# Kernel tuning notes

Hardware: AMD Instinct MI355X
Metric: run time of the kernel (lower is better)

Reference implementation:

```python
import jax, jax.numpy as jnp
import numpy as np

N, K, C = 128, 64, 64

def _w(key, shape, scale):
    return (jax.random.normal(key, shape, dtype=jnp.float32) * scale)

def setup_inputs() -> dict:
    key = jax.random.key(0)
    ks = jax.random.split(key, 20)
    s1 = 1.0 / np.sqrt(C)
    s2 = 1.0 / np.sqrt(2 * C)
    inp = {
        "x": jax.random.normal(ks[0], (N, K, C), dtype=jnp.float32),
        "W_lin": _w(ks[1], (C, C), s1), "b_lin": jnp.zeros((C,), jnp.float32),
        # unary_passing: Linear(C,C) -> tanh -> Linear(C,C)
        "Wu1": _w(ks[2], (C, C), s1), "bu1": jnp.zeros((C,), jnp.float32),
        "Wu2": _w(ks[3], (C, C), s1), "bu2": jnp.zeros((C,), jnp.float32),
        # unary_gate: Linear(C,C) -> tanh -> Linear(C,C) -> sigmoid
        "Wug1": _w(ks[4], (C, C), s1), "bug1": jnp.zeros((C,), jnp.float32),
        "Wug2": _w(ks[5], (C, C), s1), "bug2": jnp.zeros((C,), jnp.float32),
        # binary_passing: Linear(2C,C) -> tanh -> Linear(C,C)
        "Wb1": _w(ks[6], (2 * C, C), s2), "bb1": jnp.zeros((C,), jnp.float32),
        "Wb2": _w(ks[7], (C, C), s1), "bb2": jnp.zeros((C,), jnp.float32),
        # binary_gate: Linear(2C,C) -> tanh -> Linear(C,C) -> sigmoid
        "Wbg1": _w(ks[8], (2 * C, C), s2), "bbg1": jnp.zeros((C,), jnp.float32),
        "Wbg2": _w(ks[9], (C, C), s1), "bbg2": jnp.zeros((C,), jnp.float32),
        "t": 0,  # time scalar, ignored by IgnoreLinear base layer
    }
    return inp


def reference(x, W_lin, b_lin, Wu1, bu1, Wu2, bu2, Wug1, bug1, Wug2, bug2,
              Wb1, bb1, Wb2, bb2, Wbg1, bbg1, Wbg2, bbg2, t):
    # base linear map (IgnoreLinear: ignores t)
    h = x @ W_lin + b_lin                          # (N, K, C)
    n, k, c = h.shape
    # unary message with gate
    um = jnp.tanh(h @ Wu1 + bu1) @ Wu2 + bu2
    ug = jax.nn.sigmoid(jnp.tanh(h @ Wug1 + bug1) @ Wug2 + bug2)
    um = um * ug                                   # (N, K, C)
    # all-pairs broadcast-concat: hm[n,i,j] = [h[n,j], h[n,i]]
    hm = jnp.concatenate([
        jnp.broadcast_to(h[:, None, :, :], (n, k, k, c)),
        jnp.broadcast_to(h[:, :, None, :], (n, k, k, c)),
    ], axis=3)                                     # (N, K, K, 2C)
    bm = jnp.tanh(hm @ Wb1 + bb1) @ Wb2 + bb2      # (N, K, K, C)
    bg = jax.nn.sigmoid(jnp.tanh(hm @ Wbg1 + bbg1) @ Wbg2 + bbg2)
    # sum over axis 1 (includes diagonal, as in original), normalize by K-1
    bm = jnp.sum(bm * bg, axis=1) / jnp.float32(k - 1)  # (N, K, C)
    return um + bm
```

## Files before the change

kernel.cpp:

```cpp
#include <hip/hip_runtime.h>

#define S_ELEM 524288
#define WST 72

typedef __attribute__((ext_vector_type(4))) float    f32x4;
typedef __attribute__((ext_vector_type(2))) float    f32x2;
typedef __attribute__((ext_vector_type(8))) _Float16 f16x8;
typedef __attribute__((ext_vector_type(2))) _Float16 f16x2;

__device__ __forceinline__ float rcp_f(float x) { return __builtin_amdgcn_rcpf(x); }
__device__ __forceinline__ float fast_sigmoid(float x) {
    return rcp_f(1.0f + __expf(-x));
}
__device__ __forceinline__ float tanh_exp(float x) {
    return 1.0f - 2.0f * rcp_f(__expf(2.0f * x) + 1.0f);
}

__device__ __forceinline__ void read_afrag(const _Float16* Act, int row, int qd,
                                           f16x8 a[2]) {
    a[0] = *(const f16x8*)(Act + row * WST + qd * 8);
    a[1] = *(const f16x8*)(Act + row * WST + 32 + qd * 8);
}

__device__ __forceinline__ void mfma_gemm(const f16x8 a[2], const _Float16* Wt,
                                          int l16, int qd, f32x4 acc[4]) {
#pragma unroll
    for (int cc = 0; cc < 4; ++cc) {
        const _Float16* wr = Wt + (cc * 16 + l16) * WST + qd * 8;
        f16x8 b0 = *(const f16x8*)(wr);
        f16x8 b1 = *(const f16x8*)(wr + 32);
        acc[cc] = __builtin_amdgcn_mfma_f32_16x16x32_f16(a[0], b0, acc[cc], 0, 0, 0);
        acc[cc] = __builtin_amdgcn_mfma_f32_16x16x32_f16(a[1], b1, acc[cc], 0, 0, 0);
    }
}

__device__ __forceinline__ void stage_weight(const float* __restrict__ W,
                                             _Float16* Wt, int tid) {
#pragma unroll
    for (int i = 0; i < 16; ++i) {
        int idx = tid + i * 256;
        int k = idx >> 6, n = idx & 63;
        Wt[n * WST + k] = (_Float16)W[idx];
    }
}

__global__ __launch_bounds__(256) void fused_prep_kernel(
    const float* __restrict__ x,
    const float* __restrict__ W_lin, const float* __restrict__ b_lin,
    const float* __restrict__ Wu1,  const float* __restrict__ bu1,
    const float* __restrict__ Wu2,  const float* __restrict__ bu2,
    const float* __restrict__ Wug1, const float* __restrict__ bug1,
    const float* __restrict__ Wug2, const float* __restrict__ bug2,
    const float* __restrict__ Wb1,  const float* __restrict__ bb1,
    const float* __restrict__ Wbg1, const float* __restrict__ bbg1,
    const float* __restrict__ Wb2,  const float* __restrict__ Wbg2,
    float* __restrict__ EP,  float* __restrict__ EQ,
    float* __restrict__ EPg, float* __restrict__ EQg,
    float* __restrict__ um,  _Float16* __restrict__ wfrag)
{
    int tid = threadIdx.x;

    if (blockIdx.x >= 128) {
        int base = (blockIdx.x - 128) * 1024 + tid * 4;
#pragma unroll
        for (int u = 0; u < 4; ++u) {
            int idx = base + u;
            const float* W = (idx < 4096) ? Wb2 : Wbg2;
            int r = idx & 4095;
            int jj = r & 7, l16 = (r >> 3) & 15, qd = (r >> 7) & 3;
            int kk = (r >> 9) & 1, cc = (r >> 10) & 3;
            int k = kk * 32 + qd * 8 + jj, col = cc * 16 + l16;
            wfrag[idx] = (_Float16)W[k * 64 + col];
        }
        return;
    }

    __shared__ _Float16 Wt0[64 * WST], Wt1[64 * WST];
    __shared__ _Float16 Ax[64 * WST], Ah[64 * WST], Au[64 * WST], Agg[64 * WST];

    int w = tid >> 6, l = tid & 63, qd = l >> 4, l16 = l & 15;
    int row0 = blockIdx.x * 64;
    int myrow = 16 * w + l16;
    int orow  = 16 * w + qd * 4;

#pragma unroll
    for (int i = 0; i < 8; ++i) {
        int e = tid * 2 + i * 512;
        f32x2 v = *(const f32x2*)(x + (size_t)row0 * 64 + e);
        f16x2 p;
        p[0] = (_Float16)v[0];
        p[1] = (_Float16)v[1];
        *(f16x2*)(Ax + (e >> 6) * WST + (e & 63)) = p;
    }
    stage_weight(W_lin, Wt0, tid);
    __syncthreads();

    f32x4 acc[4];

    {
        f16x8 a[2]; read_afrag(Ax, myrow, qd, a);
#pragma unroll
        for (int cc = 0; cc < 4; ++cc) {
            float bv = b_lin[cc * 16 + l16];
            acc[cc] = (f32x4){bv, bv, bv, bv};
        }
        mfma_gemm(a, Wt0, l16, qd, acc);
#pragma unroll
        for (int cc = 0; cc < 4; ++cc)
#pragma unroll
            for (int r = 0; r < 4; ++r)
                Ah[(orow + r) * WST + cc * 16 + l16] = (_Float16)acc[cc][r];
    }
    stage_weight(Wb1, Wt1, tid);
    __syncthreads();

    f16x8 ah[2]; read_afrag(Ah, myrow, qd, ah);

#define STAGE(WTBUF, BIAS, NEXT_W, NEXT_BUF, EMIT)                         \
    {                                                                      \
        _Pragma("unroll")                                                  \
        for (int cc = 0; cc < 4; ++cc) {                                   \
            float bv = (BIAS) ? (BIAS)[cc * 16 + l16] : 0.0f;              \
            acc[cc] = (f32x4){bv, bv, bv, bv};                             \
        }                                                                  \
        mfma_gemm(ah, WTBUF, l16, qd, acc);                                \
        EMIT                                                               \
        if (NEXT_W) stage_weight(NEXT_W, NEXT_BUF, tid);                   \
        __syncthreads();                                                   \
    }

#define EMIT_EXP(DST)                                                      \
        _Pragma("unroll")                                                  \
        for (int cc = 0; cc < 4; ++cc)                                     \
            _Pragma("unroll")                                              \
            for (int r = 0; r < 4; ++r)                                    \
                DST[(size_t)(row0 + orow + r) * 64 + cc * 16 + l16] =      \
                    __expf(2.0f * acc[cc][r]);

#define EMIT_TANH(DST)                                                     \
        _Pragma("unroll")                                                  \
        for (int cc = 0; cc < 4; ++cc)                                     \
            _Pragma("unroll")                                              \
            for (int r = 0; r < 4; ++r)                                    \
                DST[(orow + r) * WST + cc * 16 + l16] =                    \
                    (_Float16)tanh_exp(acc[cc][r]);

    STAGE(Wt1, bb1,  Wb1 + 4096,  Wt0, EMIT_EXP(EP))
    STAGE(Wt0, (const float*)nullptr, Wbg1, Wt1, EMIT_EXP(EQ))
    STAGE(Wt1, bbg1, Wbg1 + 4096, Wt0, EMIT_EXP(EPg))
    STAGE(Wt0, (const float*)nullptr, Wu1,  Wt1, EMIT_EXP(EQg))
    STAGE(Wt1, bu1,  Wug1, Wt0, EMIT_TANH(Au))
    STAGE(Wt0, bug1, Wu2,  Wt1, EMIT_TANH(Agg))

    f32x4 uacc[4];
    {
        f16x8 au[2]; read_afrag(Au, myrow, qd, au);
#pragma unroll
        for (int cc = 0; cc < 4; ++cc) {
            float bv = bu2[cc * 16 + l16];
            uacc[cc] = (f32x4){bv, bv, bv, bv};
        }
        mfma_gemm(au, Wt1, l16, qd, uacc);
    }
    stage_weight(Wug2, Wt0, tid);
    __syncthreads();

    {
        f16x8 ag[2]; read_afrag(Agg, myrow, qd, ag);
#pragma unroll
        for (int cc = 0; cc < 4; ++cc) {
            float bv = bug2[cc * 16 + l16];
            acc[cc] = (f32x4){bv, bv, bv, bv};
        }
        mfma_gemm(ag, Wt0, l16, qd, acc);
#pragma unroll
        for (int cc = 0; cc < 4; ++cc)
#pragma unroll
            for (int r = 0; r < 4; ++r)
                um[(size_t)(row0 + orow + r) * 64 + cc * 16 + l16] =
                    uacc[cc][r] * fast_sigmoid(acc[cc][r]);
    }
#undef STAGE
#undef EMIT_EXP
#undef EMIT_TANH
}

__global__ __launch_bounds__(512) void binary_kernel(
    const float* __restrict__ EP,  const float* __restrict__ EQ,
    const float* __restrict__ EPg, const float* __restrict__ EQg,
    const float* __restrict__ bb2, const float* __restrict__ bbg2,
    const _Float16* __restrict__ wfrag,
    const float* __restrict__ um, float* __restrict__ out)
{
    __shared__ float Qb[8192];
    float* Qs  = Qb;
    float* Qgs = Qb + 4096;

    int tid = threadIdx.x, w = tid >> 6, l = tid & 63;
    int qd = l >> 4, l16 = l & 15;
    int n = blockIdx.y, j0 = blockIdx.x * 16;

    const float* EQn  = EQ  + (size_t)n * 4096;
    const float* EQgn = EQg + (size_t)n * 4096;
    for (int idx = tid * 4; idx < 4096; idx += 2048) {
        *(f32x4*)(Qs + idx)  = *(const f32x4*)(EQn + idx);
        *(f32x4*)(Qgs + idx) = *(const f32x4*)(EQgn + idx);
    }

    const float* Pr  = EP  + (size_t)n * 4096 + (j0 + l16) * 64;
    const float* Pgr = EPg + (size_t)n * 4096 + (j0 + l16) * 64;
    f32x4 pm[4], pg[4];
    pm[0] = *(const f32x4*)(Pr + qd * 8);
    pm[1] = *(const f32x4*)(Pr + qd * 8 + 4);
    pm[2] = *(const f32x4*)(Pr + 32 + qd * 8);
    pm[3] = *(const f32x4*)(Pr + 32 + qd * 8 + 4);
    pg[0] = *(const f32x4*)(Pgr + qd * 8);
    pg[1] = *(const f32x4*)(Pgr + qd * 8 + 4);
    pg[2] = *(const f32x4*)(Pgr + 32 + qd * 8);
    pg[3] = *(const f32x4*)(Pgr + 32 + qd * 8 + 4);

    const f16x8* wf = (const f16x8*)wfrag;
    f16x8 bwm[4][2], bwg[4][2];
#pragma unroll
    for (int cc = 0; cc < 4; ++cc)
#pragma unroll
        for (int kk = 0; kk < 2; ++kk) {
            bwm[cc][kk] = wf[cc * 128 + kk * 64 + qd * 16 + l16];
            bwg[cc][kk] = wf[512 + cc * 128 + kk * 64 + qd * 16 + l16];
        }
    float bim[4], big[4];
#pragma unroll
    for (int cc = 0; cc < 4; ++cc) {
        bim[cc] = bb2[cc * 16 + l16];
        big[cc] = bbg2[cc * 16 + l16];
    }
    f32x4 acc[4];
#pragma unroll
    for (int cc = 0; cc < 4; ++cc) acc[cc] = (f32x4){0.f, 0.f, 0.f, 0.f};
    __syncthreads();

    for (int ii = 8 * w; ii < 8 * w + 8; ++ii) {
        const float* qm = Qs  + ii * 64;
        const float* qg = Qgs + ii * 64;
        f16x8 am[2], ag[2];
#pragma unroll
        for (int kk = 0; kk < 2; ++kk) {
            int cb = kk * 32 + qd * 8;
            f32x4 qa = *(const f32x4*)(qm + cb);
            f32x4 qb = *(const f32x4*)(qm + cb + 4);
            f32x4 ha = *(const f32x4*)(qg + cb);
            f32x4 hb = *(const f32x4*)(qg + cb + 4);
#pragma unroll
            for (int t = 0; t < 4; ++t) {
                am[kk][t]     = (_Float16)(1.0f - 2.0f * rcp_f(__builtin_fmaf(pm[kk*2][t],   qa[t], 1.0f)));
                am[kk][t + 4] = (_Float16)(1.0f - 2.0f * rcp_f(__builtin_fmaf(pm[kk*2+1][t], qb[t], 1.0f)));
                ag[kk][t]     = (_Float16)(1.0f - 2.0f * rcp_f(__builtin_fmaf(pg[kk*2][t],   ha[t], 1.0f)));
                ag[kk][t + 4] = (_Float16)(1.0f - 2.0f * rcp_f(__builtin_fmaf(pg[kk*2+1][t], hb[t], 1.0f)));
            }
        }
#pragma unroll
        for (int cc = 0; cc < 4; ++cc) {
            f32x4 d = {bim[cc], bim[cc], bim[cc], bim[cc]};
            d = __builtin_amdgcn_mfma_f32_16x16x32_f16(am[0], bwm[cc][0], d, 0, 0, 0);
            d = __builtin_amdgcn_mfma_f32_16x16x32_f16(am[1], bwm[cc][1], d, 0, 0, 0);
            f32x4 e = {big[cc], big[cc], big[cc], big[cc]};
            e = __builtin_amdgcn_mfma_f32_16x16x32_f16(ag[0], bwg[cc][0], e, 0, 0, 0);
            e = __builtin_amdgcn_mfma_f32_16x16x32_f16(ag[1], bwg[cc][1], e, 0, 0, 0);
#pragma unroll
            for (int r = 0; r < 4; ++r)
                acc[cc][r] += d[r] * fast_sigmoid(e[r]);
        }
    }

    __syncthreads();
    float* Red = Qb;
#pragma unroll
    for (int cc = 0; cc < 4; ++cc)
#pragma unroll
        for (int r = 0; r < 4; ++r)
            Red[w * 1024 + (qd * 4 + r) * 64 + cc * 16 + l16] = acc[cc][r];
    __syncthreads();

    {
        int flat = tid * 2;
        f32x2 s = {0.f, 0.f};
#pragma unroll
        for (int ww = 0; ww < 8; ++ww)
            s += *(const f32x2*)(Red + ww * 1024 + flat);
        int row = flat >> 6, col = flat & 63;
        size_t g = (size_t)n * 4096 + (size_t)(j0 + row) * 64 + col;
        f32x2 u = *(const f32x2*)(um + g);
        f32x2 o;
        o[0] = u[0] + s[0] * (1.0f / 63.0f);
        o[1] = u[1] + s[1] * (1.0f / 63.0f);
        *(f32x2*)(out + g) = o;
    }
}

extern "C" void kernel_launch(void* const* d_in, const int* in_sizes, int n_in,
                              void* d_out, int out_size, void* d_ws, size_t ws_size,
                              hipStream_t stream)
{
    (void)in_sizes; (void)n_in; (void)out_size; (void)ws_size;
    const float* x     = (const float*)d_in[0];
    const float* W_lin = (const float*)d_in[1];
    const float* b_lin = (const float*)d_in[2];
    const float* Wu1   = (const float*)d_in[3];
    const float* bu1   = (const float*)d_in[4];
    const float* Wu2   = (const float*)d_in[5];
    const float* bu2   = (const float*)d_in[6];
    const float* Wug1  = (const float*)d_in[7];
    const float* bug1  = (const float*)d_in[8];
    const float* Wug2  = (const float*)d_in[9];
    const float* bug2  = (const float*)d_in[10];
    const float* Wb1   = (const float*)d_in[11];
    const float* bb1   = (const float*)d_in[12];
    const float* Wb2   = (const float*)d_in[13];
    const float* bb2   = (const float*)d_in[14];
    const float* Wbg1  = (const float*)d_in[15];
    const float* bbg1  = (const float*)d_in[16];
    const float* Wbg2  = (const float*)d_in[17];
    const float* bbg2  = (const float*)d_in[18];

    float*    ws    = (float*)d_ws;
    _Float16* wfrag = (_Float16*)ws;
    float* base = ws + 4096;
    float* EP   = base;
    float* EQ   = base + 1 * (size_t)S_ELEM;
    float* EPg  = base + 2 * (size_t)S_ELEM;
    float* EQg  = base + 3 * (size_t)S_ELEM;
    float* um   = base + 4 * (size_t)S_ELEM;

    hipLaunchKernelGGL(fused_prep_kernel, dim3(136), dim3(256), 0, stream,
        x, W_lin, b_lin, Wu1, bu1, Wu2, bu2, Wug1, bug1, Wug2, bug2,
        Wb1, bb1, Wbg1, bbg1, Wb2, Wbg2,
        EP, EQ, EPg, EQg, um, wfrag);
    hipLaunchKernelGGL(binary_kernel, dim3(4, 128), dim3(512), 0, stream,
        EP, EQ, EPg, EQg, bb2, bbg2, wfrag, um, (float*)d_out);
}
```

Measured before the change: 134.5 us.

## Fuse prep and binary kernels into one per-batch kernel with LDS intermediates

Merges the two-kernel pipeline into a single kernel. Each block handles one batch element and half of the output rows, recomputes the per-row linear, unary and binary projections, and keeps EP/EQ/um in shared memory instead of writing them to global workspace and reading them back. This removes a launch, the global round trip of several MB of intermediates, and the separate weight-fragment pass. In exchange, each batch's prep GEMMs are computed twice (once per block), the grid drops to 256 blocks of 512 threads, and about 111 KB of LDS per block may limit occupancy.

```diff
diff --git a/kernel.cpp b/kernel.cpp
--- a/kernel.cpp
+++ b/kernel.cpp
@@ -1,6 +1,5 @@
 #include <hip/hip_runtime.h>
 
-#define S_ELEM 524288
 #define WST 72
 
 typedef __attribute__((ext_vector_type(4))) float    f32x4;
@@ -16,35 +15,32 @@
     return 1.0f - 2.0f * rcp_f(__expf(2.0f * x) + 1.0f);
 }
 
-__device__ __forceinline__ void read_afrag(const _Float16* Act, int row, int qd,
-                                           f16x8 a[2]) {
-    a[0] = *(const f16x8*)(Act + row * WST + qd * 8);
-    a[1] = *(const f16x8*)(Act + row * WST + 32 + qd * 8);
-}
-
-__device__ __forceinline__ void mfma_gemm(const f16x8 a[2], const _Float16* Wt,
-                                          int l16, int qd, f32x4 acc[4]) {
-#pragma unroll
-    for (int cc = 0; cc < 4; ++cc) {
-        const _Float16* wr = Wt + (cc * 16 + l16) * WST + qd * 8;
+__device__ __forceinline__ void stage512(const float* __restrict__ W,
+                                         _Float16* Wt, int tid) {
+#pragma unroll
+    for (int i = 0; i < 8; ++i) {
+        int idx = tid + i * 512;
+        int k = idx >> 6, c = idx & 63;
+        Wt[c * WST + k] = (_Float16)W[idx];
+    }
+}
+
+__device__ __forceinline__ void gemm2(const _Float16* Act, int arow, int qd,
+                                      const _Float16* Wt, int colb,
+                                      f32x4 acc[2]) {
+    f16x8 a0 = *(const f16x8*)(Act + arow * WST + qd * 8);
+    f16x8 a1 = *(const f16x8*)(Act + arow * WST + 32 + qd * 8);
+#pragma unroll
+    for (int cc = 0; cc < 2; ++cc) {
+        const _Float16* wr = Wt + (colb + cc * 16) * WST + qd * 8;
         f16x8 b0 = *(const f16x8*)(wr);
         f16x8 b1 = *(const f16x8*)(wr + 32);
-        acc[cc] = __builtin_amdgcn_mfma_f32_16x16x32_f16(a[0], b0, acc[cc], 0, 0, 0);
-        acc[cc] = __builtin_amdgcn_mfma_f32_16x16x32_f16(a[1], b1, acc[cc], 0, 0, 0);
-    }
-}
-
-__device__ __forceinline__ void stage_weight(const float* __restrict__ W,
-                                             _Float16* Wt, int tid) {
-#pragma unroll
-    for (int i = 0; i < 16; ++i) {
-        int idx = tid + i * 256;
-        int k = idx >> 6, n = idx & 63;
-        Wt[n * WST + k] = (_Float16)W[idx];
-    }
-}
-
-__global__ __launch_bounds__(256) void fused_prep_kernel(
+        acc[cc] = __builtin_amdgcn_mfma_f32_16x16x32_f16(a0, b0, acc[cc], 0, 0, 0);
+        acc[cc] = __builtin_amdgcn_mfma_f32_16x16x32_f16(a1, b1, acc[cc], 0, 0, 0);
+    }
+}
+
+__global__ __launch_bounds__(512, 2) void fused_all_kernel(
     const float* __restrict__ x,
     const float* __restrict__ W_lin, const float* __restrict__ b_lin,
     const float* __restrict__ Wu1,  const float* __restrict__ bu1,
@@ -52,181 +48,181 @@
     const float* __restrict__ Wug1, const float* __restrict__ bug1,
     const float* __restrict__ Wug2, const float* __restrict__ bug2,
     const float* __restrict__ Wb1,  const float* __restrict__ bb1,
+    const float* __restrict__ Wb2,  const float* __restrict__ bb2,
     const float* __restrict__ Wbg1, const float* __restrict__ bbg1,
-    const float* __restrict__ Wb2,  const float* __restrict__ Wbg2,
-    float* __restrict__ EP,  float* __restrict__ EQ,
-    float* __restrict__ EPg, float* __restrict__ EQg,
-    float* __restrict__ um,  _Float16* __restrict__ wfrag)
+    const float* __restrict__ Wbg2, const float* __restrict__ bbg2,
+    float* __restrict__ out)
 {
-    int tid = threadIdx.x;
-
-    if (blockIdx.x >= 128) {
-        int base = (blockIdx.x - 128) * 1024 + tid * 4;
-#pragma unroll
-        for (int u = 0; u < 4; ++u) {
-            int idx = base + u;
-            const float* W = (idx < 4096) ? Wb2 : Wbg2;
-            int r = idx & 4095;
-            int jj = r & 7, l16 = (r >> 3) & 15, qd = (r >> 7) & 3;
-            int kk = (r >> 9) & 1, cc = (r >> 10) & 3;
-            int k = kk * 32 + qd * 8 + jj, col = cc * 16 + l16;
-            wfrag[idx] = (_Float16)W[k * 64 + col];
-        }
-        return;
-    }
-
-    __shared__ _Float16 Wt0[64 * WST], Wt1[64 * WST];
-    __shared__ _Float16 Ax[64 * WST], Ah[64 * WST], Au[64 * WST], Agg[64 * WST];
-
-    int w = tid >> 6, l = tid & 63, qd = l >> 4, l16 = l & 15;
-    int row0 = blockIdx.x * 64;
-    int myrow = 16 * w + l16;
-    int orow  = 16 * w + qd * 4;
-
-#pragma unroll
-    for (int i = 0; i < 8; ++i) {
-        int e = tid * 2 + i * 512;
-        f32x2 v = *(const f32x2*)(x + (size_t)row0 * 64 + e);
-        f16x2 p;
-        p[0] = (_Float16)v[0];
-        p[1] = (_Float16)v[1];
-        *(f16x2*)(Ax + (e >> 6) * WST + (e & 63)) = p;
-    }
-    stage_weight(W_lin, Wt0, tid);
-    __syncthreads();
-
-    f32x4 acc[4];
-
-    {
-        f16x8 a[2]; read_afrag(Ax, myrow, qd, a);
-#pragma unroll
-        for (int cc = 0; cc < 4; ++cc) {
-            float bv = b_lin[cc * 16 + l16];
-            acc[cc] = (f32x4){bv, bv, bv, bv};
-        }
-        mfma_gemm(a, Wt0, l16, qd, acc);
-#pragma unroll
-        for (int cc = 0; cc < 4; ++cc)
-#pragma unroll
-            for (int r = 0; r < 4; ++r)
-                Ah[(orow + r) * WST + cc * 16 + l16] = (_Float16)acc[cc][r];
-    }
-    stage_weight(Wb1, Wt1, tid);
-    __syncthreads();
-
-    f16x8 ah[2]; read_afrag(Ah, myrow, qd, ah);
-
-#define STAGE(WTBUF, BIAS, NEXT_W, NEXT_BUF, EMIT)                         \
-    {                                                                      \
-        _Pragma("unroll")                                                  \
-        for (int cc = 0; cc < 4; ++cc) {                                   \
-            float bv = (BIAS) ? (BIAS)[cc * 16 + l16] : 0.0f;              \
-            acc[cc] = (f32x4){bv, bv, bv, bv};                             \
-        }                                                                  \
-        mfma_gemm(ah, WTBUF, l16, qd, acc);                                \
-        EMIT                                                               \
-        if (NEXT_W) stage_weight(NEXT_W, NEXT_BUF, tid);                   \
-        __syncthreads();                                                   \
-    }
-
-#define EMIT_EXP(DST)                                                      \
-        _Pragma("unroll")                                                  \
-        for (int cc = 0; cc < 4; ++cc)                                     \
-            _Pragma("unroll")                                              \
-            for (int r = 0; r < 4; ++r)                                    \
-                DST[(size_t)(row0 + orow + r) * 64 + cc * 16 + l16] =      \
-                    __expf(2.0f * acc[cc][r]);
-
-#define EMIT_TANH(DST)                                                     \
-        _Pragma("unroll")                                                  \
-        for (int cc = 0; cc < 4; ++cc)                                     \
-            _Pragma("unroll")                                              \
-            for (int r = 0; r < 4; ++r)                                    \
-                DST[(orow + r) * WST + cc * 16 + l16] =                    \
-                    (_Float16)tanh_exp(acc[cc][r]);
-
-    STAGE(Wt1, bb1,  Wb1 + 4096,  Wt0, EMIT_EXP(EP))
-    STAGE(Wt0, (const float*)nullptr, Wbg1, Wt1, EMIT_EXP(EQ))
-    STAGE(Wt1, bbg1, Wbg1 + 4096, Wt0, EMIT_EXP(EPg))
-    STAGE(Wt0, (const float*)nullptr, Wu1,  Wt1, EMIT_EXP(EQg))
-    STAGE(Wt1, bu1,  Wug1, Wt0, EMIT_TANH(Au))
-    STAGE(Wt0, bug1, Wu2,  Wt1, EMIT_TANH(Agg))
-
-    f32x4 uacc[4];
-    {
-        f16x8 au[2]; read_afrag(Au, myrow, qd, au);
-#pragma unroll
-        for (int cc = 0; cc < 4; ++cc) {
-            float bv = bu2[cc * 16 + l16];
-            uacc[cc] = (f32x4){bv, bv, bv, bv};
-        }
-        mfma_gemm(au, Wt1, l16, qd, uacc);
-    }
-    stage_weight(Wug2, Wt0, tid);
-    __syncthreads();
-
-    {
-        f16x8 ag[2]; read_afrag(Agg, myrow, qd, ag);
-#pragma unroll
-        for (int cc = 0; cc < 4; ++cc) {
-            float bv = bug2[cc * 16 + l16];
-            acc[cc] = (f32x4){bv, bv, bv, bv};
-        }
-        mfma_gemm(ag, Wt0, l16, qd, acc);
-#pragma unroll
-        for (int cc = 0; cc < 4; ++cc)
-#pragma unroll
-            for (int r = 0; r < 4; ++r)
-                um[(size_t)(row0 + orow + r) * 64 + cc * 16 + l16] =
-                    uacc[cc][r] * fast_sigmoid(acc[cc][r]);
-    }
-#undef STAGE
-#undef EMIT_EXP
-#undef EMIT_TANH
-}
-
-__global__ __launch_bounds__(512) void binary_kernel(
-    const float* __restrict__ EP,  const float* __restrict__ EQ,
-    const float* __restrict__ EPg, const float* __restrict__ EQg,
-    const float* __restrict__ bb2, const float* __restrict__ bbg2,
-    const _Float16* __restrict__ wfrag,
-    const float* __restrict__ um, float* __restrict__ out)
-{
-    __shared__ float Qb[8192];
-    float* Qs  = Qb;
-    float* Qgs = Qb + 4096;
+    __shared__ __align__(16) char smem[113664];
+    _Float16* Wt0  = (_Float16*)(smem);
+    _Float16* Wt1  = (_Float16*)(smem + 9216);
+    _Float16* Ax   = (_Float16*)(smem + 18432);
+    _Float16* Ah   = (_Float16*)(smem + 27648);
+    _Float16* Au   = (_Float16*)(smem + 36864);
+    _Float16* Agg  = (_Float16*)(smem + 46080);
+    float*    EQb  = (float*)(smem + 55296);
+    float*    EQgb = (float*)(smem + 71680);
+    float*    EPm  = (float*)(smem + 88064);
+    float*    EPgm = (float*)(smem + 96768);
+    float*    um32 = (float*)(smem + 105472);
+    float*    Red  = (float*)(smem);
 
     int tid = threadIdx.x, w = tid >> 6, l = tid & 63;
     int qd = l >> 4, l16 = l & 15;
-    int n = blockIdx.y, j0 = blockIdx.x * 16;
-
-    const float* EQn  = EQ  + (size_t)n * 4096;
-    const float* EQgn = EQg + (size_t)n * 4096;
-    for (int idx = tid * 4; idx < 4096; idx += 2048) {
-        *(f32x4*)(Qs + idx)  = *(const f32x4*)(EQn + idx);
-        *(f32x4*)(Qgs + idx) = *(const f32x4*)(EQgn + idx);
-    }
-
-    const float* Pr  = EP  + (size_t)n * 4096 + (j0 + l16) * 64;
-    const float* Pgr = EPg + (size_t)n * 4096 + (j0 + l16) * 64;
-    f32x4 pm[4], pg[4];
-    pm[0] = *(const f32x4*)(Pr + qd * 8);
-    pm[1] = *(const f32x4*)(Pr + qd * 8 + 4);
-    pm[2] = *(const f32x4*)(Pr + 32 + qd * 8);
-    pm[3] = *(const f32x4*)(Pr + 32 + qd * 8 + 4);
-    pg[0] = *(const f32x4*)(Pgr + qd * 8);
-    pg[1] = *(const f32x4*)(Pgr + qd * 8 + 4);
-    pg[2] = *(const f32x4*)(Pgr + 32 + qd * 8);
-    pg[3] = *(const f32x4*)(Pgr + 32 + qd * 8 + 4);
-
-    const f16x8* wf = (const f16x8*)wfrag;
+    int n = blockIdx.x >> 1, jsel = blockIdx.x & 1;
+
+    int rw = w & 3, ch = w >> 2;
+    int arow = rw * 16 + l16;
+    int colb = ch * 32 + l16;
+    int crow = rw * 16 + qd * 4;
+    bool mine = (rw >> 1) == jsel;
+    int lr0 = (rw & 1) * 16 + qd * 4;
+
+    f32x4 acc[2];
+
+#pragma unroll
+    for (int i = 0; i < 4; ++i) {
+        int e = tid * 2 + i * 1024;
+        f32x2 v = *(const f32x2*)(x + (size_t)n * 4096 + e);
+        f16x2 p; p[0] = (_Float16)v[0]; p[1] = (_Float16)v[1];
+        *(f16x2*)(Ax + (e >> 6) * WST + (e & 63)) = p;
+    }
+    stage512(W_lin, Wt0, tid);
+    __syncthreads();
+
+#pragma unroll
+    for (int cc = 0; cc < 2; ++cc) {
+        float bv = b_lin[colb + cc * 16];
+        acc[cc] = (f32x4){bv, bv, bv, bv};
+    }
+    gemm2(Ax, arow, qd, Wt0, colb, acc);
+#pragma unroll
+    for (int cc = 0; cc < 2; ++cc)
+#pragma unroll
+        for (int r = 0; r < 4; ++r)
+            Ah[(crow + r) * WST + colb + cc * 16] = (_Float16)acc[cc][r];
+    stage512(Wb1, Wt1, tid);
+    __syncthreads();
+
+#pragma unroll
+    for (int cc = 0; cc < 2; ++cc) {
+        float bv = bb1[colb + cc * 16];
+        acc[cc] = (f32x4){bv, bv, bv, bv};
+    }
+    gemm2(Ah, arow, qd, Wt1, colb, acc);
+    if (mine) {
+#pragma unroll
+        for (int cc = 0; cc < 2; ++cc)
+#pragma unroll
+            for (int r = 0; r < 4; ++r)
+                EPm[(lr0 + r) * 68 + colb + cc * 16] = __expf(2.0f * acc[cc][r]);
+    }
+    stage512(Wb1 + 4096, Wt0, tid);
+    __syncthreads();
+
+    acc[0] = (f32x4){0.f, 0.f, 0.f, 0.f};
+    acc[1] = (f32x4){0.f, 0.f, 0.f, 0.f};
+    gemm2(Ah, arow, qd, Wt0, colb, acc);
+#pragma unroll
+    for (int cc = 0; cc < 2; ++cc)
+#pragma unroll
+        for (int r = 0; r < 4; ++r)
+            EQb[(crow + r) * 64 + colb + cc * 16] = __expf(2.0f * acc[cc][r]);
+    stage512(Wbg1, Wt1, tid);
+    __syncthreads();
+
+#pragma unroll
+    for (int cc = 0; cc < 2; ++cc) {
+        float bv = bbg1[colb + cc * 16];
+        acc[cc] = (f32x4){bv, bv, bv, bv};
+    }
+    gemm2(Ah, arow, qd, Wt1, colb, acc);
+    if (mine) {
+#pragma unroll
+        for (int cc = 0; cc < 2; ++cc)
+#pragma unroll
+            for (int r = 0; r < 4; ++r)
+                EPgm[(lr0 + r) * 68 + colb + cc * 16] = __expf(2.0f * acc[cc][r]);
+    }
+    stage512(Wbg1 + 4096, Wt0, tid);
+    __syncthreads();
+
+    acc[0] = (f32x4){0.f, 0.f, 0.f, 0.f};
+    acc[1] = (f32x4){0.f, 0.f, 0.f, 0.f};
+    gemm2(Ah, arow, qd, Wt0, colb, acc);
+#pragma unroll
+    for (int cc = 0; cc < 2; ++cc)
+#pragma unroll
+        for (int r = 0; r < 4; ++r)
+            EQgb[(crow + r) * 64 + colb + cc * 16] = __expf(2.0f * acc[cc][r]);
+    stage512(Wu1, Wt1, tid);
+    __syncthreads();
+
+#pragma unroll
+    for (int cc = 0; cc < 2; ++cc) {
+        float bv = bu1[colb + cc * 16];
+        acc[cc] = (f32x4){bv, bv, bv, bv};
+    }
+    gemm2(Ah, arow, qd, Wt1, colb, acc);
+#pragma unroll
+    for (int cc = 0; cc < 2; ++cc)
+#pragma unroll
+        for (int r = 0; r < 4; ++r)
+            Au[(crow + r) * WST + colb + cc * 16] = (_Float16)tanh_exp(acc[cc][r]);
+    stage512(Wug1, Wt0, tid);
+    __syncthreads();
+
+#pragma unroll
+    for (int cc = 0; cc < 2; ++cc) {
+        float bv = bug1[colb + cc * 16];
+        acc[cc] = (f32x4){bv, bv, bv, bv};
+    }
+    gemm2(Ah, arow, qd, Wt0, colb, acc);
+#pragma unroll
+    for (int cc = 0; cc < 2; ++cc)
+#pragma unroll
+        for (int r = 0; r < 4; ++r)
+            Agg[(crow + r) * WST + colb + cc * 16] = (_Float16)tanh_exp(acc[cc][r]);
+    stage512(Wu2, Wt1, tid);
+    __syncthreads();
+
+    f32x4 uacc[2];
+#pragma unroll
+    for (int cc = 0; cc < 2; ++cc) {
+        float bv = bu2[colb + cc * 16];
+        uacc[cc] = (f32x4){bv, bv, bv, bv};
+    }
+    gemm2(Au, arow, qd, Wt1, colb, uacc);
+    stage512(Wug2, Wt0, tid);
+    __syncthreads();
+
+#pragma unroll
+    for (int cc = 0; cc < 2; ++cc) {
+        float bv = bug2[colb + cc * 16];
+        acc[cc] = (f32x4){bv, bv, bv, bv};
+    }
+    gemm2(Agg, arow, qd, Wt0, colb, acc);
+    if (mine) {
+#pragma unroll
+        for (int cc = 0; cc < 2; ++cc)
+#pragma unroll
+            for (int r = 0; r < 4; ++r)
+                um32[(lr0 + r) * 64 + colb + cc * 16] =
+                    uacc[cc][r] * fast_sigmoid(acc[cc][r]);
+    }
+    stage512(Wb2, Wt1, tid);
+    stage512(Wbg2, Au, tid);
+    __syncthreads();
+
+    int jgrp = w >> 2, iw = w & 3;
+
     f16x8 bwm[4][2], bwg[4][2];
 #pragma unroll
     for (int cc = 0; cc < 4; ++cc)
 #pragma unroll
         for (int kk = 0; kk < 2; ++kk) {
-            bwm[cc][kk] = wf[cc * 128 + kk * 64 + qd * 16 + l16];
-            bwg[cc][kk] = wf[512 + cc * 128 + kk * 64 + qd * 16 + l16];
+            bwm[cc][kk] = *(const f16x8*)(Wt1 + (cc * 16 + l16) * WST + kk * 32 + qd * 8);
+            bwg[cc][kk] = *(const f16x8*)(Au  + (cc * 16 + l16) * WST + kk * 32 + qd * 8);
         }
     float bim[4], big[4];
 #pragma unroll
@@ -234,14 +230,26 @@
         bim[cc] = bb2[cc * 16 + l16];
         big[cc] = bbg2[cc * 16 + l16];
     }
-    f32x4 acc[4];
-#pragma unroll
-    for (int cc = 0; cc < 4; ++cc) acc[cc] = (f32x4){0.f, 0.f, 0.f, 0.f};
-    __syncthreads();
-
-    for (int ii = 8 * w; ii < 8 * w + 8; ++ii) {
-        const float* qm = Qs  + ii * 64;
-        const float* qg = Qgs + ii * 64;
+
+    const float* pr  = EPm  + (jgrp * 16 + l16) * 68;
+    const float* pgr = EPgm + (jgrp * 16 + l16) * 68;
+    f32x4 pm[4], pg[4];
+    pm[0] = *(const f32x4*)(pr + qd * 8);
+    pm[1] = *(const f32x4*)(pr + qd * 8 + 4);
+    pm[2] = *(const f32x4*)(pr + 32 + qd * 8);
+    pm[3] = *(const f32x4*)(pr + 32 + qd * 8 + 4);
+    pg[0] = *(const f32x4*)(pgr + qd * 8);
+    pg[1] = *(const f32x4*)(pgr + qd * 8 + 4);
+    pg[2] = *(const f32x4*)(pgr + 32 + qd * 8);
+    pg[3] = *(const f32x4*)(pgr + 32 + qd * 8 + 4);
+
+    f32x4 bacc[4];
+#pragma unroll
+    for (int cc = 0; cc < 4; ++cc) bacc[cc] = (f32x4){0.f, 0.f, 0.f, 0.f};
+
+    for (int ii = iw * 16; ii < iw * 16 + 16; ++ii) {
+        const float* qm = EQb  + ii * 64;
+        const float* qg = EQgb + ii * 64;
         f16x8 am[2], ag[2];
 #pragma unroll
         for (int kk = 0; kk < 2; ++kk) {
@@ -268,32 +276,32 @@
             e = __builtin_amdgcn_mfma_f32_16x16x32_f16(ag[1], bwg[cc][1], e, 0, 0, 0);
 #pragma unroll
             for (int r = 0; r < 4; ++r)
-                acc[cc][r] += d[r] * fast_sigmoid(e[r]);
+                bacc[cc][r] += d[r] * fast_sigmoid(e[r]);
         }
     }
 
     __syncthreads();
-    float* Red = Qb;
 #pragma unroll
     for (int cc = 0; cc < 4; ++cc)
 #pragma unroll
         for (int r = 0; r < 4; ++r)
-            Red[w * 1024 + (qd * 4 + r) * 64 + cc * 16 + l16] = acc[cc][r];
+            Red[(jgrp * 4 + iw) * 1024 + (qd * 4 + r) * 64 + cc * 16 + l16] = bacc[cc][r];
     __syncthreads();
 
     {
-        int flat = tid * 2;
-        f32x2 s = {0.f, 0.f};
-#pragma unroll
-        for (int ww = 0; ww < 8; ++ww)
-            s += *(const f32x2*)(Red + ww * 1024 + flat);
-        int row = flat >> 6, col = flat & 63;
-        size_t g = (size_t)n * 4096 + (size_t)(j0 + row) * 64 + col;
-        f32x2 u = *(const f32x2*)(um + g);
-        f32x2 o;
-        o[0] = u[0] + s[0] * (1.0f / 63.0f);
-        o[1] = u[1] + s[1] * (1.0f / 63.0f);
-        *(f32x2*)(out + g) = o;
+        int e = tid * 4;
+        int lr = e >> 6, col = e & 63;
+        int g = lr >> 4, rr = lr & 15;
+        f32x4 s = {0.f, 0.f, 0.f, 0.f};
+#pragma unroll
+        for (int w2 = 0; w2 < 4; ++w2)
+            s += *(const f32x4*)(Red + (g * 4 + w2) * 1024 + rr * 64 + col);
+        f32x4 u = *(const f32x4*)(um32 + lr * 64 + col);
+        f32x4 o;
+#pragma unroll
+        for (int t = 0; t < 4; ++t)
+            o[t] = u[t] + s[t] * (1.0f / 63.0f);
+        *(f32x4*)(out + (size_t)n * 4096 + (size_t)(jsel * 32 + lr) * 64 + col) = o;
     }
 }
 
@@ -301,7 +309,7 @@
                               void* d_out, int out_size, void* d_ws, size_t ws_size,
                               hipStream_t stream)
 {
-    (void)in_sizes; (void)n_in; (void)out_size; (void)ws_size;
+    (void)in_sizes; (void)n_in; (void)out_size; (void)d_ws; (void)ws_size;
     const float* x     = (const float*)d_in[0];
     const float* W_lin = (const float*)d_in[1];
     const float* b_lin = (const float*)d_in[2];
@@ -322,19 +330,8 @@
     const float* Wbg2  = (const float*)d_in[17];
     const float* bbg2  = (const float*)d_in[18];
 
-    float*    ws    = (float*)d_ws;
-    _Float16* wfrag = (_Float16*)ws;
-    float* base = ws + 4096;
-    float* EP   = base;
-    float* EQ   = base + 1 * (size_t)S_ELEM;
-    float* EPg  = base + 2 * (size_t)S_ELEM;
-    float* EQg  = base + 3 * (size_t)S_ELEM;
-    float* um   = base + 4 * (size_t)S_ELEM;
-
-    hipLaunchKernelGGL(fused_prep_kernel, dim3(136), dim3(256), 0, stream,
+    hipLaunchKernelGGL(fused_all_kernel, dim3(256), dim3(512), 0, stream,
         x, W_lin, b_lin, Wu1, bu1, Wu2, bu2, Wug1, bug1, Wug2, bug2,
-        Wb1, bb1, Wbg1, bbg1, Wb2, Wbg2,
-        EP, EQ, EPg, EQg, um, wfrag);
-    hipLaunchKernelGGL(binary_kernel, dim3(4, 128), dim3(512), 0, stream,
-        EP, EQ, EPg, EQg, bb2, bbg2, wfrag, um, (float*)d_out);
-}
+        Wb1, bb1, Wb2, bb2, Wbg1, bbg1, Wbg2, bbg2,
+        (float*)d_out);
+}
```

Measured after the change: 116.7 us. 1.15x faster.
